# Kernel tuning notes

Hardware: AMD Instinct MI355X
Metric: run time of the kernel (lower is better)

## Reference

```python
import jax, jax.numpy as jnp
import numpy as np

EPS = 1e-7
MAX_NORM = 1.0 - 1e-5  # Poincare ball (c=1) projection radius
NUM_NODES = 50000
NUM_EDGES = 800000
NUM_GRAPHS = 512
D_IN = 64
D_H = 64
D_OUT = 16


def _norm(x):
    return jnp.clip(jnp.linalg.norm(x, axis=-1, keepdims=True), EPS)


def expmap0(u):
    n = _norm(u)
    return jnp.tanh(n) * u / n


def logmap0(x):
    n = _norm(x)
    nc = jnp.clip(n, EPS, MAX_NORM)
    return jnp.arctanh(nc) * x / n


def proj(x):
    n = _norm(x)
    return jnp.where(n > MAX_NORM, x * (MAX_NORM / n), x)


def mobius_add(x, y):
    x2 = jnp.sum(x * x, axis=-1, keepdims=True)
    y2 = jnp.sum(y * y, axis=-1, keepdims=True)
    xy = jnp.sum(x * y, axis=-1, keepdims=True)
    num = (1.0 + 2.0 * xy + y2) * x + (1.0 - x2) * y
    den = jnp.clip(1.0 + 2.0 * xy + x2 * y2, EPS)
    return num / den


def hyp_linear(x, W, b):
    # mobius matvec + hyperbolic bias add
    h = proj(expmap0(logmap0(x) @ W.T))
    hb = proj(expmap0(b))
    return proj(mobius_add(h, hb))


def hyp_agg(x, src, dst, num_nodes):
    # mean aggregation of neighbor messages in the tangent space at the origin
    xt = logmap0(x)                                   # [N, d]
    msg = xt[src]                                     # [E, d] gather
    s = jax.ops.segment_sum(msg, dst, num_segments=num_nodes)
    cnt = jax.ops.segment_sum(jnp.ones((msg.shape[0],), xt.dtype), dst,
                              num_segments=num_nodes)
    agg = s / jnp.clip(cnt, 1.0)[:, None]
    return proj(expmap0(agg))


def hyp_act(x, act):
    return proj(expmap0(act(logmap0(x))))


def hgcn_layer(x, W, b, src, dst, num_nodes, act):
    h = hyp_linear(x, W, b)
    h = hyp_agg(h, src, dst, num_nodes)
    if act is not None:
        h = hyp_act(h, act)
    return h


def setup_inputs() -> dict:
    key = jax.random.key(0)
    ks = jax.random.split(key, 12)
    x = jax.random.normal(ks[0], (NUM_NODES, D_IN), jnp.float32) * 0.1
    edge_index = jax.random.randint(ks[1], (2, NUM_EDGES), 0, NUM_NODES, jnp.int64 if jax.config.jax_enable_x64 else jnp.int32)
    batch = jnp.sort(jax.random.randint(ks[2], (NUM_NODES,), 0, NUM_GRAPHS))
    def w(k, o, i):
        return jax.random.normal(k, (o, i), jnp.float32) * (1.0 / np.sqrt(i))
    return {
        "x": x,
        "W1": w(ks[3], D_H, D_IN), "b1": jnp.zeros((D_H,), jnp.float32),
        "W2": w(ks[4], D_H, D_H),  "b2": jnp.zeros((D_H,), jnp.float32),
        "W3": w(ks[5], D_H, D_H),  "b3": jnp.zeros((D_H,), jnp.float32),
        "W4": w(ks[6], D_OUT, D_H), "b4": jnp.zeros((D_OUT,), jnp.float32),
        "edge_index": edge_index,
        "batch": batch,
    }


def reference(x, W1, b1, W2, b2, W3, b3, W4, b4, edge_index, batch):
    act = lambda v: jax.nn.leaky_relu(v, 0.2)
    n = x.shape[0]
    src, dst = edge_index[0], edge_index[1]
    h = proj(expmap0(x))
    h = hgcn_layer(h, W1, b1, src, dst, n, act)
    h = hgcn_layer(h, W2, b2, src, dst, n, act)
    h = hgcn_layer(h, W3, b3, src, dst, n, None)
    t = logmap0(h)
    # global mean pool over graphs (eval-mode dropout = identity)
    s = jax.ops.segment_sum(t, batch, num_segments=NUM_GRAPHS)
    cnt = jax.ops.segment_sum(jnp.ones((n,), t.dtype), batch, num_segments=NUM_GRAPHS)
    pooled = s / jnp.clip(cnt, 1.0)[:, None]            # [G, d]
    h = proj(expmap0(pooled))
    out = hyp_linear(h, W4, b4)                          # HNNLayer, no activation
    return out
```

## Files before the change

### kernel.cpp

```cpp
#include <hip/hip_runtime.h>
#include <hip/hip_fp16.h>

#define EPSF 1e-7f
#define MAXNORM (1.0f - 1e-5f)

__device__ __forceinline__ float rsum64(float v) {
#pragma unroll
  for (int m = 32; m; m >>= 1) v += __shfl_xor(v, m, 64);
  return v;
}
__device__ __forceinline__ float rsum16(float v) {
#pragma unroll
  for (int m = 8; m; m >>= 1) v += __shfl_xor(v, m, 64);
  return v;
}
__device__ __forceinline__ float gr8(float v) {
  v += __shfl_xor(v, 1, 64);
  v += __shfl_xor(v, 2, 64);
  v += __shfl_xor(v, 4, 64);
  return v;
}

__device__ __forceinline__ float frcp(float x) { return __builtin_amdgcn_rcpf(x); }
__device__ __forceinline__ float fsqrt_(float x) { return __builtin_amdgcn_sqrtf(x); }
__device__ __forceinline__ float tanh_fast(float x) {
  x = fminf(x, 20.f);
  float e = __builtin_amdgcn_exp2f(x * 2.88539008178f);
  return (e - 1.f) * frcp(e + 1.f);
}
__device__ __forceinline__ float atanh_fast(float x) {
  return 0.34657359028f * __builtin_amdgcn_logf((1.f + x) * frcp(1.f - x));
}
__device__ __forceinline__ float lp_exp_log_scale(float nu) {
  float te = tanh_fast(nu);
  float tec = fminf(fmaxf(te, EPSF), MAXNORM);
  return atanh_fast(tec) * frcp(fmaxf(te, EPSF)) * te * frcp(nu);
}

__device__ __forceinline__ float4 ld4(const float* p) {
  return *reinterpret_cast<const float4*>(p);
}

__device__ __forceinline__ void gather8h(const int* __restrict__ csr,
                                         const __half* __restrict__ xtp,
                                         int r0, int deg, int g, int sub,
                                         float acc[8]) {
  const uint4* xt4 = reinterpret_cast<const uint4*>(xtp);
  for (int j0 = 0; j0 < deg; j0 += 8) {
    int myidx = 0;
    if (j0 + sub < deg) myidx = csr[r0 + j0 + sub];
#pragma unroll
    for (int m = 0; m < 8; ++m) {
      int idx = __shfl(myidx, (g << 3) | m, 64);
      float msk = (j0 + m < deg) ? 1.f : 0.f;
      union { uint4 u; __half2 h[4]; } U;
      U.u = xt4[(size_t)idx * 8 + sub];
      float2 f0 = __half22float2(U.h[0]);
      float2 f1 = __half22float2(U.h[1]);
      float2 f2 = __half22float2(U.h[2]);
      float2 f3 = __half22float2(U.h[3]);
      acc[0] = fmaf(msk, f0.x, acc[0]); acc[1] = fmaf(msk, f0.y, acc[1]);
      acc[2] = fmaf(msk, f1.x, acc[2]); acc[3] = fmaf(msk, f1.y, acc[3]);
      acc[4] = fmaf(msk, f2.x, acc[4]); acc[5] = fmaf(msk, f2.y, acc[5]);
      acc[6] = fmaf(msk, f3.x, acc[6]); acc[7] = fmaf(msk, f3.y, acc[7]);
    }
  }
}

__device__ __forceinline__ void st8h(__half* __restrict__ xt, int node, int sub,
                                     const float o[8]) {
  union { uint4 u; __half2 h[4]; } U;
  U.h[0] = __floats2half2_rn(o[0], o[1]);
  U.h[1] = __floats2half2_rn(o[2], o[3]);
  U.h[2] = __floats2half2_rn(o[4], o[5]);
  U.h[3] = __floats2half2_rn(o[6], o[7]);
  reinterpret_cast<uint4*>(xt)[(size_t)node * 8 + sub] = U.u;
}

__device__ __forceinline__ void linear_tail8(
    const float* __restrict__ Wl, float* __restrict__ sc, int g, int sub,
    int lane, const float t2[8], const float hb8[8], float hb2, float out8[8]) {
  float4* sw = reinterpret_cast<float4*>(sc + g * 68 + sub * 8);
  sw[0] = make_float4(t2[0], t2[1], t2[2], t2[3]);
  sw[1] = make_float4(t2[4], t2[5], t2[6], t2[7]);
  float y[8] = {0.f, 0.f, 0.f, 0.f, 0.f, 0.f, 0.f, 0.f};
  const float4* Wrow = reinterpret_cast<const float4*>(Wl + lane * 68);
#pragma unroll
  for (int q = 0; q < 16; ++q) {
    float4 w = Wrow[q];
#pragma unroll
    for (int g2 = 0; g2 < 8; ++g2) {
      float4 tq = *reinterpret_cast<const float4*>(sc + g2 * 68 + q * 4);
      y[g2] = fmaf(w.x, tq.x, fmaf(w.y, tq.y, fmaf(w.z, tq.z, fmaf(w.w, tq.w, y[g2]))));
    }
  }
#pragma unroll
  for (int g2 = 0; g2 < 8; ++g2) sc[g2 * 68 + lane] = y[g2];
  float4 r0 = *reinterpret_cast<const float4*>(sc + g * 68 + sub * 8);
  float4 r1 = *reinterpret_cast<const float4*>(sc + g * 68 + sub * 8 + 4);
  float yv[8] = {r0.x, r0.y, r0.z, r0.w, r1.x, r1.y, r1.z, r1.w};
  float p1 = 0.f, p2 = 0.f;
#pragma unroll
  for (int j = 0; j < 8; ++j) {
    p1 = fmaf(yv[j], yv[j], p1);
    p2 = fmaf(yv[j], hb8[j], p2);
  }
  p1 = gr8(p1); p2 = gr8(p2);
  float ny = fmaxf(fsqrt_(p1), EPSF);
  float cy = fminf(tanh_fast(ny), MAXNORM);
  float k = cy * frcp(ny);
  float xy = k * p2;
  float x2 = cy * cy;
  float aa = 1.f + 2.f * xy + hb2;
  float cc = 1.f - x2;
  float den = fmaxf(1.f + 2.f * xy + x2 * hb2, EPSF);
  float rd = frcp(den);
  float nr2 = (aa * aa * x2 + 2.f * aa * cc * xy + cc * cc * hb2) * rd * rd;
  float nr = fmaxf(fsqrt_(nr2), EPSF);
  float s = atanh_fast(fminf(nr, MAXNORM)) * frcp(nr);
  float sk = s * rd;
#pragma unroll
  for (int j = 0; j < 8; ++j) out8[j] = sk * (aa * k * yv[j] + cc * hb8[j]);
}

__global__ void k_hist8(const int* __restrict__ dst, int* __restrict__ deg8,
                        int E, int N) {
  int e = blockIdx.x * blockDim.x + threadIdx.x;
  if (e >= E) return;
  int c = blockIdx.x & 7;
  atomicAdd(&deg8[(size_t)c * N + dst[e]], 1);
}

__global__ void __launch_bounds__(256) k_red8(int* __restrict__ deg8,
                                              int* __restrict__ offs8,
                                              int* __restrict__ deg, int N) {
  int d = blockIdx.x * blockDim.x + threadIdx.x;
  if (d >= N) return;
  int s = 0;
#pragma unroll
  for (int k = 0; k < 8; ++k) {
    int v = deg8[(size_t)k * N + d];
    offs8[(size_t)k * N + d] = s;
    s += v;
  }
  deg[d] = s;
}

__global__ void __launch_bounds__(256) k_scanA(const int* __restrict__ deg,
                                               int* __restrict__ locscan,
                                               int* __restrict__ partial, int N) {
  __shared__ int buf[256];
  int i = blockIdx.x * 256 + threadIdx.x;
  int v = (i < N) ? deg[i] : 0;
  buf[threadIdx.x] = v;
  __syncthreads();
#pragma unroll
  for (int off = 1; off < 256; off <<= 1) {
    int t = (threadIdx.x >= off) ? buf[threadIdx.x - off] : 0;
    __syncthreads();
    buf[threadIdx.x] += t;
    __syncthreads();
  }
  if (i < N) locscan[i] = buf[threadIdx.x] - v;
  if (threadIdx.x == 255) partial[blockIdx.x] = buf[255];
}

__global__ void __launch_bounds__(256) k_scanB(int* __restrict__ partial, int nb) {
  __shared__ int buf[256];
  int v = (threadIdx.x < nb) ? partial[threadIdx.x] : 0;
  buf[threadIdx.x] = v;
  __syncthreads();
#pragma unroll
  for (int off = 1; off < 256; off <<= 1) {
    int t = (threadIdx.x >= off) ? buf[threadIdx.x - off] : 0;
    __syncthreads();
    buf[threadIdx.x] += t;
    __syncthreads();
  }
  if (threadIdx.x < nb) partial[threadIdx.x] = buf[threadIdx.x] - v;
}

__global__ void __launch_bounds__(256) k_scanC(const int* __restrict__ locscan,
                                               const int* __restrict__ partial,
                                               int* __restrict__ rowptr, int N, int E) {
  int i = blockIdx.x * 256 + threadIdx.x;
  if (i < N) rowptr[i] = locscan[i] + partial[blockIdx.x];
  if (i == 0) rowptr[N] = E;
}

__global__ void k_fill8(const int* __restrict__ src, const int* __restrict__ dst,
                        const int* __restrict__ rowptr,
                        const int* __restrict__ offs8, int* __restrict__ deg8,
                        int* __restrict__ csr, int E, int N) {
  int e = blockIdx.x * blockDim.x + threadIdx.x;
  if (e >= E) return;
  int c = blockIdx.x & 7;
  int d = dst[e];
  int p = atomicSub(&deg8[(size_t)c * N + d], 1) - 1;
  csr[rowptr[d] + offs8[(size_t)c * N + d] + p] = src[e];
}

__global__ void k_gsize(const int* __restrict__ batch, float* __restrict__ cntg,
                        int N, int G) {
  int g = blockIdx.x * blockDim.x + threadIdx.x;
  if (g >= G) return;
  int lo = 0, hi = N;
  while (lo < hi) { int mid = (lo + hi) >> 1; if (batch[mid] < g) lo = mid + 1; else hi = mid; }
  int lb = lo;
  lo = 0; hi = N; int g1 = g + 1;
  while (lo < hi) { int mid = (lo + hi) >> 1; if (batch[mid] < g1) lo = mid + 1; else hi = mid; }
  cntg[g] = (float)(lo - lb);
}

__global__ void __launch_bounds__(192) k_prepb(const float* __restrict__ b1,
                                               const float* __restrict__ b2,
                                               const float* __restrict__ b3,
                                               float* __restrict__ hb_all,
                                               float* __restrict__ hb2_all) {
  int w = threadIdx.x >> 6, lane = threadIdx.x & 63;
  const float* b = (w == 0) ? b1 : (w == 1) ? b2 : b3;
  float bb = b[lane];
  float nb = fmaxf(fsqrt_(rsum64(bb * bb)), EPSF);
  float tb = tanh_fast(nb);
  float cb = fminf(tb, MAXNORM);
  float hb = cb * frcp(nb) * bb;
  hb_all[w * 64 + lane] = hb;
  if (lane == 0) hb2_all[w] = cb * cb;
}

__global__ void __launch_bounds__(512) k_lin1(const float* __restrict__ x,
                                              const float* __restrict__ W,
                                              const float* __restrict__ hb,
                                              const float* __restrict__ hb2p,
                                              __half* __restrict__ xt, int N) {
  __shared__ __align__(16) float Wl[64 * 68];
  __shared__ __align__(16) float sc_all[8][8 * 68];
  int tid = threadIdx.x, wid = tid >> 6, lane = tid & 63;
  int g = lane >> 3, sub = lane & 7;
  for (int i = tid; i < 4096; i += 512) Wl[(i >> 6) * 68 + (i & 63)] = W[i];
  __syncthreads();
  float hb2 = hb2p[0];
  float4 h0 = ld4(hb + sub * 8), h1 = ld4(hb + sub * 8 + 4);
  float hb8[8] = {h0.x, h0.y, h0.z, h0.w, h1.x, h1.y, h1.z, h1.w};

  int slot = blockIdx.x * 64 + wid * 8 + g;
  bool valid = slot < N;
  int node = valid ? slot : 0;
  const float* row = x + (size_t)node * 64 + sub * 8;
  float4 v0 = ld4(row), v1 = ld4(row + 4);
  float xa[8] = {v0.x, v0.y, v0.z, v0.w, v1.x, v1.y, v1.z, v1.w};
  float p = 0.f;
#pragma unroll
  for (int j = 0; j < 8; ++j) p = fmaf(xa[j], xa[j], p);
  p = gr8(p);
  float na = fmaxf(fsqrt_(p), EPSF);
  float sc1 = lp_exp_log_scale(na);
  float t2[8];
#pragma unroll
  for (int j = 0; j < 8; ++j) t2[j] = sc1 * xa[j];
  float out8[8];
  linear_tail8(Wl, sc_all[wid], g, sub, lane, t2, hb8, hb2, out8);
  if (valid) st8h(xt, node, sub, out8);
}

__global__ void __launch_bounds__(512) k_gatherlin(
    const int* __restrict__ rowptr, const int* __restrict__ csr,
    const __half* __restrict__ xtp, const float* __restrict__ W,
    const float* __restrict__ hb, const float* __restrict__ hb2p,
    __half* __restrict__ xt, int N) {
  __shared__ __align__(16) float Wl[64 * 68];
  __shared__ __align__(16) float sc_all[8][8 * 68];
  int tid = threadIdx.x, wid = tid >> 6, lane = tid & 63;
  int g = lane >> 3, sub = lane & 7;
  for (int i = tid; i < 4096; i += 512) Wl[(i >> 6) * 68 + (i & 63)] = W[i];
  __syncthreads();
  float hb2 = hb2p[0];
  float4 h0 = ld4(hb + sub * 8), h1 = ld4(hb + sub * 8 + 4);
  float hb8[8] = {h0.x, h0.y, h0.z, h0.w, h1.x, h1.y, h1.z, h1.w};

  int slot = blockIdx.x * 64 + wid * 8 + g;
  bool valid = slot < N;
  int node = valid ? slot : 0;
  int r0 = rowptr[node];
  int deg = valid ? (rowptr[node + 1] - r0) : 0;
  float acc[8] = {0.f, 0.f, 0.f, 0.f, 0.f, 0.f, 0.f, 0.f};
  gather8h(csr, xtp, r0, deg, g, sub, acc);
  float rdeg = frcp(fmaxf((float)deg, 1.f));
  float u[8];
#pragma unroll
  for (int j = 0; j < 8; ++j) u[j] = acc[j] * rdeg;
  float p = 0.f, q = 0.f;
#pragma unroll
  for (int j = 0; j < 8; ++j) {
    float w = (u[j] < 0.f) ? 0.04f : 1.f;
    p = fmaf(u[j], u[j], p);
    q = fmaf(w * u[j], u[j], q);
  }
  p = gr8(p); q = gr8(q);
  float nu = fmaxf(fsqrt_(p), EPSF);
  float s1 = lp_exp_log_scale(nu);
  float nt = fmaxf(s1 * fsqrt_(q), EPSF);
  float f = lp_exp_log_scale(nt) * s1;
  float t2[8];
#pragma unroll
  for (int j = 0; j < 8; ++j) t2[j] = f * u[j] * ((u[j] < 0.f) ? 0.2f : 1.f);
  float out8[8];
  linear_tail8(Wl, sc_all[wid], g, sub, lane, t2, hb8, hb2, out8);
  if (valid) st8h(xt, node, sub, out8);
}

__global__ void __launch_bounds__(512) k_gpool(const int* __restrict__ rowptr,
                                               const int* __restrict__ csr,
                                               const __half* __restrict__ xtp,
                                               const int* __restrict__ batch,
                                               float* __restrict__ pooled, int N) {
  int tid = threadIdx.x, wid = tid >> 6, lane = tid & 63;
  int g = lane >> 3, sub = lane & 7;
  int slot = blockIdx.x * 64 + wid * 8 + g;
  bool valid = slot < N;
  int node = valid ? slot : 0;
  int r0 = rowptr[node];
  int deg = valid ? (rowptr[node + 1] - r0) : 0;
  float acc[8] = {0.f, 0.f, 0.f, 0.f, 0.f, 0.f, 0.f, 0.f};
  gather8h(csr, xtp, r0, deg, g, sub, acc);
  float rdeg = frcp(fmaxf((float)deg, 1.f));
  float u[8], p = 0.f;
#pragma unroll
  for (int j = 0; j < 8; ++j) {
    u[j] = acc[j] * rdeg;
    p = fmaf(u[j], u[j], p);
  }
  p = gr8(p);
  float nu = fmaxf(fsqrt_(p), EPSF);
  float s = lp_exp_log_scale(nu);
  float t8[8];
#pragma unroll
  for (int j = 0; j < 8; ++j) t8[j] = (valid ? s : 0.f) * u[j];
  int bs = batch[node];
  int b0 = __shfl(bs, 0, 64);
  bool uniform = __all(valid && bs == b0);
  if (uniform) {
#pragma unroll
    for (int j = 0; j < 8; ++j) {
      t8[j] += __shfl_xor(t8[j], 8, 64);
      t8[j] += __shfl_xor(t8[j], 16, 64);
      t8[j] += __shfl_xor(t8[j], 32, 64);
    }
    if (g == 0) {
#pragma unroll
      for (int j = 0; j < 8; ++j)
        atomicAdd(&pooled[(size_t)b0 * 64 + sub * 8 + j], t8[j]);
    }
  } else if (valid) {
#pragma unroll
    for (int j = 0; j < 8; ++j)
      atomicAdd(&pooled[(size_t)bs * 64 + sub * 8 + j], t8[j]);
  }
}

__global__ void __launch_bounds__(64) k_final(const float* __restrict__ pooled,
                                              const float* __restrict__ cntg,
                                              const float* __restrict__ W4,
                                              const float* __restrict__ b4,
                                              float* __restrict__ out, int G) {
  int g = blockIdx.x;
  int lane = threadIdx.x;
  float u = pooled[(size_t)g * 64 + lane] / fmaxf(cntg[g], 1.0f);
  float n = fmaxf(sqrtf(rsum64(u * u)), EPSF);
  float e = tanhf(n) * u / n;
  float ne = fmaxf(sqrtf(rsum64(e * e)), EPSF);
  if (ne > MAXNORM) e *= MAXNORM / ne;
  float nn = fmaxf(sqrtf(rsum64(e * e)), EPSF);
  float t = atanhf(fminf(nn, MAXNORM)) * e / nn;

  int row = lane & 15;
  float acc = 0.f;
#pragma unroll
  for (int k = 0; k < 64; ++k) {
    float tk = __shfl(t, k, 64);
    acc = fmaf(W4[row * 64 + k], tk, acc);
  }
  float ny = fmaxf(sqrtf(rsum16(acc * acc)), EPSF);
  float hy = tanhf(ny) * acc / ny;
  float nh = fmaxf(sqrtf(rsum16(hy * hy)), EPSF);
  if (nh > MAXNORM) hy *= MAXNORM / nh;
  float bb = b4[row];
  float nb = fmaxf(sqrtf(rsum16(bb * bb)), EPSF);
  float hb = tanhf(nb) * bb / nb;
  float nhb = fmaxf(sqrtf(rsum16(hb * hb)), EPSF);
  if (nhb > MAXNORM) hb *= MAXNORM / nhb;
  float x2 = rsum16(hy * hy);
  float y2 = rsum16(hb * hb);
  float xy = rsum16(hy * hb);
  float num = (1.f + 2.f * xy + y2) * hy + (1.f - x2) * hb;
  float den = fmaxf(1.f + 2.f * xy + x2 * y2, EPSF);
  float r = num / den;
  float nr = fmaxf(sqrtf(rsum16(r * r)), EPSF);
  if (nr > MAXNORM) r *= MAXNORM / nr;
  if (lane < 16) out[(size_t)g * 16 + lane] = r;
}

extern "C" void kernel_launch(void* const* d_in, const int* in_sizes, int n_in,
                              void* d_out, int out_size, void* d_ws, size_t ws_size,
                              hipStream_t stream) {
  const float* x  = (const float*)d_in[0];
  const float* W1 = (const float*)d_in[1];
  const float* b1 = (const float*)d_in[2];
  const float* W2 = (const float*)d_in[3];
  const float* b2 = (const float*)d_in[4];
  const float* W3 = (const float*)d_in[5];
  const float* b3 = (const float*)d_in[6];
  const float* W4 = (const float*)d_in[7];
  const float* b4 = (const float*)d_in[8];
  const int* ei   = (const int*)d_in[9];
  const int* batch = (const int*)d_in[10];

  int N = in_sizes[0] / 64;
  int E = in_sizes[9] / 2;
  int G = out_size / 16;
  const int* src = ei;
  const int* dst = ei + E;

  float* ws = (float*)d_ws;
  __half* xtA   = (__half*)ws;
  __half* xtB   = xtA + (size_t)N * 64;
  float* pooled = ws + (size_t)N * 64;
  float* cntg   = pooled + (size_t)G * 64;
  float* hb_all = cntg + G;
  float* hb2_all = hb_all + 192;
  int* ip       = (int*)(hb2_all + 4);
  int* deg      = ip;
  int* locscan  = deg + N;
  int* rowptr   = locscan + N;
  int* partial  = rowptr + N + 1;
  int* deg8     = partial + 256;
  int* offs8    = deg8 + (size_t)8 * N;
  int* csr      = offs8 + (size_t)8 * N;
  float* out = (float*)d_out;

  int nbN = (N + 255) / 256;
  int nbE = (E + 255) / 256;
  int nb64 = (N + 63) / 64;

  hipMemsetAsync(deg8, 0, (size_t)8 * N * sizeof(int), stream);
  hipMemsetAsync(pooled, 0, (size_t)G * 64 * sizeof(float), stream);

  k_hist8<<<nbE, 256, 0, stream>>>(dst, deg8, E, N);
  k_gsize<<<(G + 255) / 256, 256, 0, stream>>>(batch, cntg, N, G);
  k_red8<<<nbN, 256, 0, stream>>>(deg8, offs8, deg, N);
  k_scanA<<<nbN, 256, 0, stream>>>(deg, locscan, partial, N);
  k_scanB<<<1, 256, 0, stream>>>(partial, nbN);
  k_scanC<<<nbN, 256, 0, stream>>>(locscan, partial, rowptr, N, E);
  k_fill8<<<nbE, 256, 0, stream>>>(src, dst, rowptr, offs8, deg8, csr, E, N);

  k_prepb<<<1, 192, 0, stream>>>(b1, b2, b3, hb_all, hb2_all);

  k_lin1<<<nb64, 512, 0, stream>>>(x, W1, hb_all, hb2_all, xtA, N);
  k_gatherlin<<<nb64, 512, 0, stream>>>(rowptr, csr, xtA, W2, hb_all + 64,
                                        hb2_all + 1, xtB, N);
  k_gatherlin<<<nb64, 512, 0, stream>>>(rowptr, csr, xtB, W3, hb_all + 128,
                                        hb2_all + 2, xtA, N);
  k_gpool<<<nb64, 512, 0, stream>>>(rowptr, csr, xtA, batch, pooled, N);
  k_final<<<G, 64, 0, stream>>>(pooled, cntg, W4, b4, out, G);
}
```

Before: 210.2 us.

## Use chunk-major CSR with 16-bit neighbor indices and drop degree reduction

The CSR build now scans all 8 per-chunk degree histograms directly into a chunk-major row-pointer array of size 8N. This removes the separate per-node reduction kernel and the offset array. The scan-partials kernel loops so it can handle more than 256 blocks. Neighbor indices are stored as unsigned 16-bit values to halve CSR traffic. In exchange, each gather resolves a node's 8 chunk segments with shuffles and selects, and there is no check or fallback for node counts above 65535.

```diff
diff --git a/kernel.cpp b/kernel.cpp
--- a/kernel.cpp
+++ b/kernel.cpp
@@ -41,17 +41,38 @@
   return *reinterpret_cast<const float4*>(p);
 }
 
-__device__ __forceinline__ void gather8h(const int* __restrict__ csr,
-                                         const __half* __restrict__ xtp,
-                                         int r0, int deg, int g, int sub,
-                                         float acc[8]) {
+__device__ __forceinline__ int gather8h_cm(const unsigned short* __restrict__ csr,
+                                           const int* __restrict__ rowptr8,
+                                           int N, int d, const __half* __restrict__ xtp,
+                                           int g, int sub, int lane, float acc[8]) {
   const uint4* xt4 = reinterpret_cast<const uint4*>(xtp);
+  int base_s = rowptr8[(size_t)sub * N + d];
+  int cnt_s = rowptr8[(size_t)sub * N + d + 1] - base_s;
+  int lb = lane & 56;
+  int c0 = __shfl(cnt_s, lb + 0, 64), c1 = __shfl(cnt_s, lb + 1, 64);
+  int c2 = __shfl(cnt_s, lb + 2, 64), c3 = __shfl(cnt_s, lb + 3, 64);
+  int c4 = __shfl(cnt_s, lb + 4, 64), c5 = __shfl(cnt_s, lb + 5, 64);
+  int c6 = __shfl(cnt_s, lb + 6, 64), c7 = __shfl(cnt_s, lb + 7, 64);
+  int b0 = __shfl(base_s, lb + 0, 64), b1 = __shfl(base_s, lb + 1, 64);
+  int b2 = __shfl(base_s, lb + 2, 64), b3 = __shfl(base_s, lb + 3, 64);
+  int b4 = __shfl(base_s, lb + 4, 64), b5 = __shfl(base_s, lb + 5, 64);
+  int b6 = __shfl(base_s, lb + 6, 64), b7 = __shfl(base_s, lb + 7, 64);
+  int p1 = c0, p2 = p1 + c1, p3 = p2 + c2, p4 = p3 + c3;
+  int p5 = p4 + c4, p6 = p5 + c5, p7 = p6 + c6;
+  int deg = p7 + c7;
+  int s0 = b0, s1 = b1 - p1, s2 = b2 - p2, s3 = b3 - p3;
+  int s4 = b4 - p4, s5 = b5 - p5, s6 = b6 - p6, s7 = b7 - p7;
   for (int j0 = 0; j0 < deg; j0 += 8) {
-    int myidx = 0;
-    if (j0 + sub < deg) myidx = csr[r0 + j0 + sub];
+    int j = j0 + sub;
+    int s = s0;
+    s = (j >= p1) ? s1 : s; s = (j >= p2) ? s2 : s;
+    s = (j >= p3) ? s3 : s; s = (j >= p4) ? s4 : s;
+    s = (j >= p5) ? s5 : s; s = (j >= p6) ? s6 : s;
+    s = (j >= p7) ? s7 : s;
+    int myidx = (j < deg) ? (int)csr[s + j] : 0;
 #pragma unroll
     for (int m = 0; m < 8; ++m) {
-      int idx = __shfl(myidx, (g << 3) | m, 64);
+      int idx = __shfl(myidx, lb + m, 64);
       float msk = (j0 + m < deg) ? 1.f : 0.f;
       union { uint4 u; __half2 h[4]; } U;
       U.u = xt4[(size_t)idx * 8 + sub];
@@ -65,6 +86,7 @@
       acc[6] = fmaf(msk, f3.x, acc[6]); acc[7] = fmaf(msk, f3.y, acc[7]);
     }
   }
+  return deg;
 }
 
 __device__ __forceinline__ void st8h(__half* __restrict__ xt, int node, int sub,
@@ -131,27 +153,12 @@
   atomicAdd(&deg8[(size_t)c * N + dst[e]], 1);
 }
 
-__global__ void __launch_bounds__(256) k_red8(int* __restrict__ deg8,
-                                              int* __restrict__ offs8,
-                                              int* __restrict__ deg, int N) {
-  int d = blockIdx.x * blockDim.x + threadIdx.x;
-  if (d >= N) return;
-  int s = 0;
-#pragma unroll
-  for (int k = 0; k < 8; ++k) {
-    int v = deg8[(size_t)k * N + d];
-    offs8[(size_t)k * N + d] = s;
-    s += v;
-  }
-  deg[d] = s;
-}
-
 __global__ void __launch_bounds__(256) k_scanA(const int* __restrict__ deg,
                                                int* __restrict__ locscan,
-                                               int* __restrict__ partial, int N) {
+                                               int* __restrict__ partial, int M) {
   __shared__ int buf[256];
   int i = blockIdx.x * 256 + threadIdx.x;
-  int v = (i < N) ? deg[i] : 0;
+  int v = (i < M) ? deg[i] : 0;
   buf[threadIdx.x] = v;
   __syncthreads();
 #pragma unroll
@@ -161,43 +168,50 @@
     buf[threadIdx.x] += t;
     __syncthreads();
   }
-  if (i < N) locscan[i] = buf[threadIdx.x] - v;
+  if (i < M) locscan[i] = buf[threadIdx.x] - v;
   if (threadIdx.x == 255) partial[blockIdx.x] = buf[255];
 }
 
 __global__ void __launch_bounds__(256) k_scanB(int* __restrict__ partial, int nb) {
   __shared__ int buf[256];
-  int v = (threadIdx.x < nb) ? partial[threadIdx.x] : 0;
-  buf[threadIdx.x] = v;
-  __syncthreads();
-#pragma unroll
-  for (int off = 1; off < 256; off <<= 1) {
-    int t = (threadIdx.x >= off) ? buf[threadIdx.x - off] : 0;
+  int carry = 0;
+  for (int base = 0; base < nb; base += 256) {
+    int i = base + threadIdx.x;
+    int v = (i < nb) ? partial[i] : 0;
+    buf[threadIdx.x] = v;
     __syncthreads();
-    buf[threadIdx.x] += t;
+#pragma unroll
+    for (int off = 1; off < 256; off <<= 1) {
+      int t = (threadIdx.x >= off) ? buf[threadIdx.x - off] : 0;
+      __syncthreads();
+      buf[threadIdx.x] += t;
+      __syncthreads();
+    }
+    if (i < nb) partial[i] = carry + buf[threadIdx.x] - v;
+    int total = buf[255];
     __syncthreads();
-  }
-  if (threadIdx.x < nb) partial[threadIdx.x] = buf[threadIdx.x] - v;
+    carry += total;
+  }
 }
 
 __global__ void __launch_bounds__(256) k_scanC(const int* __restrict__ locscan,
                                                const int* __restrict__ partial,
-                                               int* __restrict__ rowptr, int N, int E) {
+                                               int* __restrict__ rowptr8, int M, int E) {
   int i = blockIdx.x * 256 + threadIdx.x;
-  if (i < N) rowptr[i] = locscan[i] + partial[blockIdx.x];
-  if (i == 0) rowptr[N] = E;
-}
-
-__global__ void k_fill8(const int* __restrict__ src, const int* __restrict__ dst,
-                        const int* __restrict__ rowptr,
-                        const int* __restrict__ offs8, int* __restrict__ deg8,
-                        int* __restrict__ csr, int E, int N) {
+  if (i < M) rowptr8[i] = locscan[i] + partial[blockIdx.x];
+  if (i == 0) rowptr8[M] = E;
+}
+
+__global__ void k_fillc(const int* __restrict__ src, const int* __restrict__ dst,
+                        const int* __restrict__ rowptr8, int* __restrict__ deg8,
+                        unsigned short* __restrict__ csr, int E, int N) {
   int e = blockIdx.x * blockDim.x + threadIdx.x;
   if (e >= E) return;
   int c = blockIdx.x & 7;
   int d = dst[e];
-  int p = atomicSub(&deg8[(size_t)c * N + d], 1) - 1;
-  csr[rowptr[d] + offs8[(size_t)c * N + d] + p] = src[e];
+  size_t k = (size_t)c * N + d;
+  int p = atomicSub(&deg8[k], 1) - 1;
+  csr[rowptr8[k] + p] = (unsigned short)src[e];
 }
 
 __global__ void k_gsize(const int* __restrict__ batch, float* __restrict__ cntg,
@@ -264,7 +278,7 @@
 }
 
 __global__ void __launch_bounds__(512) k_gatherlin(
-    const int* __restrict__ rowptr, const int* __restrict__ csr,
+    const int* __restrict__ rowptr8, const unsigned short* __restrict__ csr,
     const __half* __restrict__ xtp, const float* __restrict__ W,
     const float* __restrict__ hb, const float* __restrict__ hb2p,
     __half* __restrict__ xt, int N) {
@@ -281,10 +295,8 @@
   int slot = blockIdx.x * 64 + wid * 8 + g;
   bool valid = slot < N;
   int node = valid ? slot : 0;
-  int r0 = rowptr[node];
-  int deg = valid ? (rowptr[node + 1] - r0) : 0;
   float acc[8] = {0.f, 0.f, 0.f, 0.f, 0.f, 0.f, 0.f, 0.f};
-  gather8h(csr, xtp, r0, deg, g, sub, acc);
+  int deg = gather8h_cm(csr, rowptr8, N, node, xtp, g, sub, lane, acc);
   float rdeg = frcp(fmaxf((float)deg, 1.f));
   float u[8];
 #pragma unroll
@@ -309,8 +321,8 @@
   if (valid) st8h(xt, node, sub, out8);
 }
 
-__global__ void __launch_bounds__(512) k_gpool(const int* __restrict__ rowptr,
-                                               const int* __restrict__ csr,
+__global__ void __launch_bounds__(512) k_gpool(const int* __restrict__ rowptr8,
+                                               const unsigned short* __restrict__ csr,
                                                const __half* __restrict__ xtp,
                                                const int* __restrict__ batch,
                                                float* __restrict__ pooled, int N) {
@@ -319,10 +331,8 @@
   int slot = blockIdx.x * 64 + wid * 8 + g;
   bool valid = slot < N;
   int node = valid ? slot : 0;
-  int r0 = rowptr[node];
-  int deg = valid ? (rowptr[node + 1] - r0) : 0;
   float acc[8] = {0.f, 0.f, 0.f, 0.f, 0.f, 0.f, 0.f, 0.f};
-  gather8h(csr, xtp, r0, deg, g, sub, acc);
+  int deg = gather8h_cm(csr, rowptr8, N, node, xtp, g, sub, lane, acc);
   float rdeg = frcp(fmaxf((float)deg, 1.f));
   float u[8], p = 0.f;
 #pragma unroll
@@ -429,37 +439,35 @@
   float* hb_all = cntg + G;
   float* hb2_all = hb_all + 192;
   int* ip       = (int*)(hb2_all + 4);
-  int* deg      = ip;
-  int* locscan  = deg + N;
-  int* rowptr   = locscan + N;
-  int* partial  = rowptr + N + 1;
-  int* deg8     = partial + 256;
-  int* offs8    = deg8 + (size_t)8 * N;
-  int* csr      = offs8 + (size_t)8 * N;
+  int* deg8     = ip;
+  int* locscan  = deg8 + (size_t)8 * N;
+  int* rowptr8  = locscan + (size_t)8 * N;
+  int* partial  = rowptr8 + (size_t)8 * N + 8;
+  unsigned short* csr = (unsigned short*)(partial + 2048);
   float* out = (float*)d_out;
 
-  int nbN = (N + 255) / 256;
+  int M = 8 * N;
+  int nbM = (M + 255) / 256;
   int nbE = (E + 255) / 256;
   int nb64 = (N + 63) / 64;
 
-  hipMemsetAsync(deg8, 0, (size_t)8 * N * sizeof(int), stream);
+  hipMemsetAsync(deg8, 0, (size_t)M * sizeof(int), stream);
   hipMemsetAsync(pooled, 0, (size_t)G * 64 * sizeof(float), stream);
 
   k_hist8<<<nbE, 256, 0, stream>>>(dst, deg8, E, N);
   k_gsize<<<(G + 255) / 256, 256, 0, stream>>>(batch, cntg, N, G);
-  k_red8<<<nbN, 256, 0, stream>>>(deg8, offs8, deg, N);
-  k_scanA<<<nbN, 256, 0, stream>>>(deg, locscan, partial, N);
-  k_scanB<<<1, 256, 0, stream>>>(partial, nbN);
-  k_scanC<<<nbN, 256, 0, stream>>>(locscan, partial, rowptr, N, E);
-  k_fill8<<<nbE, 256, 0, stream>>>(src, dst, rowptr, offs8, deg8, csr, E, N);
+  k_scanA<<<nbM, 256, 0, stream>>>(deg8, locscan, partial, M);
+  k_scanB<<<1, 256, 0, stream>>>(partial, nbM);
+  k_scanC<<<nbM, 256, 0, stream>>>(locscan, partial, rowptr8, M, E);
+  k_fillc<<<nbE, 256, 0, stream>>>(src, dst, rowptr8, deg8, csr, E, N);
 
   k_prepb<<<1, 192, 0, stream>>>(b1, b2, b3, hb_all, hb2_all);
 
   k_lin1<<<nb64, 512, 0, stream>>>(x, W1, hb_all, hb2_all, xtA, N);
-  k_gatherlin<<<nb64, 512, 0, stream>>>(rowptr, csr, xtA, W2, hb_all + 64,
+  k_gatherlin<<<nb64, 512, 0, stream>>>(rowptr8, csr, xtA, W2, hb_all + 64,
                                         hb2_all + 1, xtB, N);
-  k_gatherlin<<<nb64, 512, 0, stream>>>(rowptr, csr, xtB, W3, hb_all + 128,
+  k_gatherlin<<<nb64, 512, 0, stream>>>(rowptr8, csr, xtB, W3, hb_all + 128,
                                         hb2_all + 2, xtA, N);
-  k_gpool<<<nb64, 512, 0, stream>>>(rowptr, csr, xtA, batch, pooled, N);
+  k_gpool<<<nb64, 512, 0, stream>>>(rowptr8, csr, xtA, batch, pooled, N);
   k_final<<<G, 64, 0, stream>>>(pooled, cntg, W4, b4, out, G);
 }
```

Result: slower. 218.8 us (+4.1%).
